# Optimization experiments

Hardware: AMD Instinct MI355X
Metric: run time of the kernel (lower is better)

## Reference

```python
import jax, jax.numpy as jnp
import numpy as np

N = 50000          # nodes
E = 1600000        # edges (avg degree 32)
B = 64             # graphs in batch
D_NODE = 128
D_EDGE = 64
D_EMB = 128
D_HID = 2 * D_EMB  # GCN output channels
EPS = 1e-5


def setup_inputs() -> dict:
    key = jax.random.key(0)
    ks = jax.random.split(key, 12)
    g = lambda k, shape: jax.random.normal(k, shape, jnp.float32) * (shape[0] ** -0.5)
    return {
        "x": jax.random.normal(ks[0], (N, D_NODE), jnp.float32),
        "edge_attr": jax.random.normal(ks[1], (E, D_EDGE), jnp.float32),
        "edge_index": jax.random.randint(ks[2], (2, E), 0, N),
        "batch": jnp.sort(jax.random.randint(ks[3], (N,), 0, B)),
        # GCNConv params
        "W1": g(ks[4], (D_NODE, D_HID)), "b1": jnp.zeros((D_HID,), jnp.float32),
        # TransformerConv params (heads=1)
        "Wq": g(ks[5], (D_HID, D_EMB)), "bq": jnp.zeros((D_EMB,), jnp.float32),
        "Wk": g(ks[6], (D_HID, D_EMB)), "bk": jnp.zeros((D_EMB,), jnp.float32),
        "Wv": g(ks[7], (D_HID, D_EMB)), "bv": jnp.zeros((D_EMB,), jnp.float32),
        "We": g(ks[8], (D_EDGE, D_EMB)), "be": jnp.zeros((D_EMB,), jnp.float32),
        "Wr": g(ks[9], (D_HID, D_EMB)), "br": jnp.zeros((D_EMB,), jnp.float32),
        # LayerNorm params
        "gamma": jnp.ones((D_EMB,), jnp.float32), "beta": jnp.zeros((D_EMB,), jnp.float32),
    }


def _forward(x, edge_attr, edge_index, batch,
             W1, b1, Wq, bq, Wk, bk, Wv, bv, We, be, Wr, br, gamma, beta):
    src, dst = edge_index[0], edge_index[1]

    # ---- GCNConv: symmetric normalization with self-loops ----
    xw = x @ W1                                                # [N, D_HID]
    deg = 1.0 + jax.ops.segment_sum(jnp.ones((E,), x.dtype), dst, num_segments=N)
    dinv = jax.lax.rsqrt(deg)                                  # deg >= 1
    norm = dinv[src] * dinv[dst]                               # [E]
    agg = jax.ops.segment_sum(xw[src] * norm[:, None], dst, num_segments=N)
    h = agg + xw * (dinv * dinv)[:, None] + b1                 # self-loop term
    h = jax.nn.relu(h)                                         # dropout = identity (eval)

    # ---- TransformerConv (heads=1, edge_dim) ----
    q = h @ Wq + bq                                            # [N, D_EMB]
    k = h @ Wk + bk
    v = h @ Wv + bv
    e = edge_attr @ We + be                                    # [E, D_EMB]
    k_j = k[src] + e
    v_j = v[src] + e
    logits = jnp.sum(q[dst] * k_j, axis=-1) / jnp.sqrt(jnp.float32(D_EMB))  # [E]
    # segment softmax over incoming edges of each target node
    lmax = jax.ops.segment_max(logits, dst, num_segments=N)
    exp_l = jnp.exp(logits - lmax[dst])
    denom = jax.ops.segment_sum(exp_l, dst, num_segments=N)
    alpha = exp_l / denom[dst]                                 # [E]
    out = jax.ops.segment_sum(alpha[:, None] * v_j, dst, num_segments=N)
    out = out + h @ Wr + br                                    # root/skip connection

    # ---- LayerNorm + ReLU ----
    mu = jnp.mean(out, axis=-1, keepdims=True)
    var = jnp.var(out, axis=-1, keepdims=True)
    out = (out - mu) * jax.lax.rsqrt(var + EPS) * gamma + beta
    out = jax.nn.relu(out)

    # ---- global mean pool over graphs ----
    sums = jax.ops.segment_sum(out, batch, num_segments=B)     # [B, D_EMB]
    cnts = jax.ops.segment_sum(jnp.ones((N,), out.dtype), batch, num_segments=B)
    return sums / jnp.maximum(cnts, 1.0)[:, None]


def reference(x, edge_attr, edge_index, batch,
              W1, b1, Wq, bq, Wk, bk, Wv, bv, We, be, Wr, br, gamma, beta):
    return _forward(x, edge_attr, edge_index, batch,
                    W1, b1, Wq, bq, Wk, bk, Wv, bv, We, be, Wr, br, gamma, beta)
```

## Files before the change

kernel.cpp:

```cpp
#include <hip/hip_runtime.h>

typedef short bf16x8 __attribute__((ext_vector_type(8)));
typedef float f32x4 __attribute__((ext_vector_type(4)));

#define DN 128
#define DE 64
#define DEMB 128
#define DHID 256
#define SCALE 0.08838834764831845f

__device__ __forceinline__ ushort f2bf(float f) {
  unsigned u = __float_as_uint(f);
  return (ushort)((u + 0x7FFFu + ((u >> 16) & 1u)) >> 16);
}
__device__ __forceinline__ float bf2f(ushort u) {
  return __uint_as_float((unsigned)u << 16);
}

__global__ void k_prep1(const float* __restrict__ W1, ushort* __restrict__ Wp1) {
  int idx = blockIdx.x * 256 + threadIdx.x;
  if (idx >= 16 * 4 * 64 * 8) return;
  int j = idx & 7, lane = (idx >> 3) & 63, s = (idx >> 9) & 3, t = idx >> 11;
  int k = s * 32 + (lane >> 4) * 8 + j;
  int c = t * 16 + (lane & 15);
  Wp1[idx] = f2bf(W1[k * DHID + c]);
}

__global__ void k_prep2(const float* __restrict__ Wq, const float* __restrict__ Wk,
                        const float* __restrict__ Wv, const float* __restrict__ Wr,
                        const float* __restrict__ We, ushort* __restrict__ Wp2) {
  int idx = blockIdx.x * 256 + threadIdx.x;
  if (idx >= 36 * 8 * 64 * 8) return;
  int j = idx & 7, lane = (idx >> 3) & 63, s = (idx >> 9) & 7, t = idx >> 12;
  int k = s * 32 + (lane >> 4) * 8 + j;
  int c = t * 16 + (lane & 15);
  float v;
  if (c < 128)       v = Wq[k * DEMB + c] * SCALE;
  else if (c < 256)  v = Wk[k * DEMB + (c - 128)];
  else if (c < 384)  v = Wv[k * DEMB + (c - 256)];
  else if (c < 512)  v = Wr[k * DEMB + (c - 384)];
  else {
    int cc = c - 512;
    float a = 0.f;
    for (int u = 0; u < DEMB; ++u) a += Wq[k * DEMB + u] * We[cc * DEMB + u];
    v = a * SCALE;
  }
  Wp2[idx] = f2bf(v);
}

__global__ void k_prep_b(const float* __restrict__ bq, const float* __restrict__ bk,
                         const float* __restrict__ bv, const float* __restrict__ br,
                         const float* __restrict__ be, const float* __restrict__ We,
                         float* __restrict__ bcat) {
  int j = blockIdx.x * 256 + threadIdx.x;
  if (j >= 576) return;
  float v;
  if (j < 128)       v = bq[j] * SCALE;
  else if (j < 256)  v = bk[j - 128] + be[j - 128];
  else if (j < 384)  v = bv[j - 256] + be[j - 256];
  else if (j < 512)  v = br[j - 384];
  else {
    int cc = j - 512;
    float a = 0.f;
    for (int u = 0; u < DEMB; ++u) a += bq[u] * We[cc * DEMB + u];
    v = a * SCALE;
  }
  bcat[j] = v;
}

__global__ void k_prep3(const float* __restrict__ We, ushort* __restrict__ Wp3) {
  int idx = blockIdx.x * 256 + threadIdx.x;
  if (idx >= 8 * 2 * 64 * 8) return;
  int j = idx & 7, lane = (idx >> 3) & 63, s = (idx >> 9) & 1, t = idx >> 10;
  int k = s * 32 + (lane >> 4) * 8 + j;
  int c = t * 16 + (lane & 15);
  Wp3[idx] = f2bf(We[k * DEMB + c]);
}

__global__ void k_deg(const int* __restrict__ ei, int* __restrict__ degi, int nE) {
  int e = blockIdx.x * 256 + threadIdx.x;
  if (e < nE) atomicAdd(&degi[ei[nE + e]], 1);
}

__global__ void k_dinv(const int* __restrict__ degi, float* __restrict__ dinv, int nN) {
  int n = blockIdx.x * 256 + threadIdx.x;
  if (n < nN) dinv[n] = rsqrtf(1.0f + (float)degi[n]);
}

__global__ __launch_bounds__(1024) void k_scan(const int* __restrict__ degi,
                                               int* __restrict__ row_ptr, int n) {
  __shared__ int wsum[16];
  __shared__ int carry_s;
  int lane = threadIdx.x & 63, wid = threadIdx.x >> 6;
  if (threadIdx.x == 0) carry_s = 0;
  __syncthreads();
  for (int base = 0; base < n; base += 1024) {
    int i = base + threadIdx.x;
    int v = (i < n) ? degi[i] : 0;
    int sc = v;
    #pragma unroll
    for (int off = 1; off < 64; off <<= 1) {
      int t = __shfl_up(sc, off);
      if (lane >= off) sc += t;
    }
    if (lane == 63) wsum[wid] = sc;
    int carry0 = carry_s;
    __syncthreads();
    if (wid == 0) {
      int w = (lane < 16) ? wsum[lane] : 0;
      int swc = w;
      #pragma unroll
      for (int off = 1; off < 16; off <<= 1) {
        int t = __shfl_up(swc, off);
        if (lane >= off) swc += t;
      }
      if (lane < 16) wsum[lane] = swc - w;
      if (lane == 15) carry_s = carry0 + swc;
    }
    __syncthreads();
    if (i < n) row_ptr[i] = carry0 + wsum[wid] + sc - v;
    __syncthreads();
  }
  if (threadIdx.x == 0) row_ptr[n] = carry_s;
}

__global__ void k_scatter(const int* __restrict__ ei, const int* __restrict__ row_ptr,
                          int* __restrict__ cursor, int2* __restrict__ csr_se, int nE) {
  int e = blockIdx.x * 256 + threadIdx.x;
  if (e >= nE) return;
  int dst = ei[nE + e];
  int pos = row_ptr[dst] + atomicAdd(&cursor[dst], 1);
  csr_se[pos] = make_int2(ei[e], e);
}

__global__ void k_gbounds(const int* __restrict__ batch, int* __restrict__ gstart,
                          int nN, int B) {
  int n = blockIdx.x * 256 + threadIdx.x;
  if (n >= nN) return;
  int b = batch[n];
  if (n == 0) {
    for (int g = 0; g <= b; ++g) gstart[g] = 0;
  } else {
    int pb = batch[n - 1];
    for (int g = pb + 1; g <= b; ++g) gstart[g] = n;
  }
  if (n == nN - 1) {
    for (int g = b + 1; g <= B; ++g) gstart[g] = nN;
  }
}

__global__ __launch_bounds__(256) void k_gemm1(const float* __restrict__ x,
                                               const ushort* __restrict__ Wp1,
                                               const float* __restrict__ dinv,
                                               ushort* __restrict__ xwsb, int nN) {
  int lane = threadIdx.x & 63, wave = threadIdx.x >> 6;
  int l15 = lane & 15, lh = lane >> 4;
  int m0 = blockIdx.x * 16;
  int rowa = m0 + l15; if (rowa >= nN) rowa = nN - 1;
  f32x4 acc[4] = {};
  for (int s = 0; s < 4; ++s) {
    const float* ap = &x[(size_t)rowa * DN + s * 32 + lh * 8];
    float4 a0 = *(const float4*)ap;
    float4 a1 = *(const float4*)(ap + 4);
    bf16x8 af;
    af[0] = (short)f2bf(a0.x); af[1] = (short)f2bf(a0.y);
    af[2] = (short)f2bf(a0.z); af[3] = (short)f2bf(a0.w);
    af[4] = (short)f2bf(a1.x); af[5] = (short)f2bf(a1.y);
    af[6] = (short)f2bf(a1.z); af[7] = (short)f2bf(a1.w);
    #pragma unroll
    for (int tt = 0; tt < 4; ++tt) {
      int t = wave * 4 + tt;
      bf16x8 bf = *(const bf16x8*)&Wp1[((t * 4 + s) * 64 + lane) * 8];
      acc[tt] = __builtin_amdgcn_mfma_f32_16x16x32_bf16(af, bf, acc[tt], 0, 0, 0);
    }
  }
  #pragma unroll
  for (int tt = 0; tt < 4; ++tt) {
    int c = (wave * 4 + tt) * 16 + l15;
    #pragma unroll
    for (int r = 0; r < 4; ++r) {
      int row = m0 + lh * 4 + r;
      if (row < nN) xwsb[(size_t)row * DHID + c] = f2bf(acc[tt][r] * dinv[row]);
    }
  }
}

__global__ __launch_bounds__(256) void k_gemm2(const ushort* __restrict__ hb,
                                               const ushort* __restrict__ Wp2,
                                               const float* __restrict__ bcat,
                                               ushort* __restrict__ qwb,
                                               ushort* __restrict__ kb,
                                               ushort* __restrict__ vb,
                                               ushort* __restrict__ hrb, int nN) {
  int lane = threadIdx.x & 63, wave = threadIdx.x >> 6;
  int l15 = lane & 15, lh = lane >> 4;
  int m0 = blockIdx.x * 16;
  int rowa = m0 + l15; if (rowa >= nN) rowa = nN - 1;
  f32x4 acc[9] = {};
  for (int s = 0; s < 8; ++s) {
    bf16x8 af = *(const bf16x8*)&hb[(size_t)rowa * DHID + s * 32 + lh * 8];
    #pragma unroll
    for (int tt = 0; tt < 9; ++tt) {
      int t = wave * 9 + tt;
      bf16x8 bf = *(const bf16x8*)&Wp2[((t * 8 + s) * 64 + lane) * 8];
      acc[tt] = __builtin_amdgcn_mfma_f32_16x16x32_bf16(af, bf, acc[tt], 0, 0, 0);
    }
  }
  #pragma unroll
  for (int tt = 0; tt < 9; ++tt) {
    int c = (wave * 9 + tt) * 16 + l15;
    float bc = bcat[c];
    #pragma unroll
    for (int r = 0; r < 4; ++r) {
      int row = m0 + lh * 4 + r;
      if (row >= nN) continue;
      ushort val = f2bf(acc[tt][r] + bc);
      if (c < 128)      qwb[(size_t)row * 192 + c] = val;
      else if (c < 256) kb[(size_t)row * 128 + (c - 128)] = val;
      else if (c < 384) vb[(size_t)row * 128 + (c - 256)] = val;
      else if (c < 512) hrb[(size_t)row * 128 + (c - 384)] = val;
      else              qwb[(size_t)row * 192 + 128 + (c - 512)] = val;
    }
  }
}

__global__ __launch_bounds__(256) void k_gcnE(const ushort* __restrict__ xwsb,
                                              const int2* __restrict__ csr_se,
                                              const int* __restrict__ row_ptr,
                                              const float* __restrict__ dinv,
                                              const float* __restrict__ b1,
                                              ushort* __restrict__ hb, int nN) {
  int lane = threadIdx.x & 63;
  int n = blockIdx.x * 4 + (threadIdx.x >> 6);
  if (n >= nN) return;
  int grp = lane >> 4, l15 = lane & 15;
  int beg = row_ptr[n], end = row_ptr[n + 1];
  float acc[16] = {};
  for (int i0 = beg; i0 < end; i0 += 8) {
    #pragma unroll
    for (int u = 0; u < 2; ++u) {
      int e = i0 + u * 4 + grp;
      bool val = e < end;
      int cl = val ? e : end - 1;
      int src = csr_se[cl].x;
      const ushort* xr = &xwsb[(size_t)src * DHID + l15 * 16];
      uint4 xa = *(const uint4*)xr;
      uint4 xb = *(const uint4*)(xr + 8);
      float w = val ? 1.f : 0.f;
      unsigned qq[8] = {xa.x, xa.y, xa.z, xa.w, xb.x, xb.y, xb.z, xb.w};
      #pragma unroll
      for (int d = 0; d < 8; ++d) {
        acc[2*d]   = fmaf(w, __uint_as_float(qq[d] << 16), acc[2*d]);
        acc[2*d+1] = fmaf(w, __uint_as_float(qq[d] & 0xFFFF0000u), acc[2*d+1]);
      }
    }
  }
  #pragma unroll
  for (int d = 0; d < 16; ++d) {
    acc[d] += __shfl_xor(acc[d], 16);
    acc[d] += __shfl_xor(acc[d], 32);
  }
  if (grp == 0) {
    const ushort* sr = &xwsb[(size_t)n * DHID + l15 * 16];
    uint4 sa = *(const uint4*)sr;
    uint4 sb = *(const uint4*)(sr + 8);
    unsigned sq[8] = {sa.x, sa.y, sa.z, sa.w, sb.x, sb.y, sb.z, sb.w};
    float dn = dinv[n];
    unsigned ov[8];
    #pragma unroll
    for (int d = 0; d < 8; ++d) {
      float blo = b1[l15 * 16 + 2*d], bhi = b1[l15 * 16 + 2*d + 1];
      float lo = __uint_as_float(sq[d] << 16);
      float hi = __uint_as_float(sq[d] & 0xFFFF0000u);
      float v0 = fmaxf((acc[2*d]   + lo) * dn + blo, 0.f);
      float v1 = fmaxf((acc[2*d+1] + hi) * dn + bhi, 0.f);
      ov[d] = (unsigned)f2bf(v0) | ((unsigned)f2bf(v1) << 16);
    }
    uint4 o0 = {ov[0], ov[1], ov[2], ov[3]};
    uint4 o1 = {ov[4], ov[5], ov[6], ov[7]};
    ushort* hr = &hb[(size_t)n * DHID + l15 * 16];
    *(uint4*)hr = o0;
    *(uint4*)(hr + 8) = o1;
  }
}

__global__ __launch_bounds__(256) void k_edge(const ushort* __restrict__ qwb,
                                              const ushort* __restrict__ kb,
                                              const ushort* __restrict__ vb,
                                              const float* __restrict__ ea32,
                                              const int2* __restrict__ csr_se,
                                              const int* __restrict__ row_ptr,
                                              float* __restrict__ sden,
                                              float* __restrict__ vaccf,
                                              ushort* __restrict__ ewb, int nN) {
  int lane = threadIdx.x & 63;
  int n = blockIdx.x * 4 + (threadIdx.x >> 6);
  if (n >= nN) return;
  int grp = lane >> 4, l15 = lane & 15;
  const ushort* qp = &qwb[(size_t)n * 192];
  bf16x8 qv = *(const bf16x8*)&qp[l15 * 8];
  ushort4 wv = *(const ushort4*)&qp[128 + l15 * 4];
  float q[8];
  #pragma unroll
  for (int d = 0; d < 8; ++d) q[d] = bf2f((ushort)qv[d]);
  float w0 = bf2f(wv.x), w1 = bf2f(wv.y), w2 = bf2f(wv.z), w3 = bf2f(wv.w);
  float s_acc = 0.f;
  float av[8] = {};
  float ae[4] = {};
  int beg = row_ptr[n], end = row_ptr[n + 1];
  for (int i0 = beg; i0 < end; i0 += 8) {
    #pragma unroll
    for (int u = 0; u < 2; ++u) {
      int e = i0 + u * 4 + grp;
      bool val = e < end;
      int cl = val ? e : end - 1;
      int2 se = csr_se[cl];
      bf16x8 kv8 = *(const bf16x8*)&kb[(size_t)se.x * 128 + l15 * 8];
      bf16x8 vv8 = *(const bf16x8*)&vb[(size_t)se.x * 128 + l15 * 8];
      float4 eav = *(const float4*)&ea32[(size_t)se.y * DE + l15 * 4];
      float dot = w0 * eav.x + w1 * eav.y + w2 * eav.z + w3 * eav.w;
      #pragma unroll
      for (int d = 0; d < 8; ++d) dot = fmaf(q[d], bf2f((ushort)kv8[d]), dot);
      dot += __shfl_xor(dot, 1);
      dot += __shfl_xor(dot, 2);
      dot += __shfl_xor(dot, 4);
      dot += __shfl_xor(dot, 8);
      float p = val ? __expf(dot) : 0.f;
      s_acc += p;
      #pragma unroll
      for (int d = 0; d < 8; ++d) av[d] = fmaf(p, bf2f((ushort)vv8[d]), av[d]);
      ae[0] = fmaf(p, eav.x, ae[0]);
      ae[1] = fmaf(p, eav.y, ae[1]);
      ae[2] = fmaf(p, eav.z, ae[2]);
      ae[3] = fmaf(p, eav.w, ae[3]);
    }
  }
  s_acc += __shfl_xor(s_acc, 16); s_acc += __shfl_xor(s_acc, 32);
  #pragma unroll
  for (int d = 0; d < 8; ++d) {
    av[d] += __shfl_xor(av[d], 16);
    av[d] += __shfl_xor(av[d], 32);
  }
  #pragma unroll
  for (int d = 0; d < 4; ++d) {
    ae[d] += __shfl_xor(ae[d], 16);
    ae[d] += __shfl_xor(ae[d], 32);
  }
  if (grp == 0) {
    if (l15 == 0) sden[n] = s_acc;
    float4 o0 = {av[0], av[1], av[2], av[3]};
    float4 o1 = {av[4], av[5], av[6], av[7]};
    float* vr = &vaccf[(size_t)n * 128 + l15 * 8];
    *(float4*)vr = o0;
    *(float4*)(vr + 4) = o1;
    ushort4 eo;
    eo.x = f2bf(ae[0]); eo.y = f2bf(ae[1]); eo.z = f2bf(ae[2]); eo.w = f2bf(ae[3]);
    *(ushort4*)&ewb[(size_t)n * DE + l15 * 4] = eo;
  }
}

__global__ __launch_bounds__(256) void k_ewe(const ushort* __restrict__ ewb,
                                             const ushort* __restrict__ Wp3,
                                             float* __restrict__ ewout, int nN) {
  int lane = threadIdx.x & 63, wave = threadIdx.x >> 6;
  int l15 = lane & 15, lh = lane >> 4;
  int m0 = blockIdx.x * 16;
  int rowa = m0 + l15; if (rowa >= nN) rowa = nN - 1;
  f32x4 acc[2] = {};
  #pragma unroll
  for (int s = 0; s < 2; ++s) {
    bf16x8 af = *(const bf16x8*)&ewb[(size_t)rowa * DE + s * 32 + lh * 8];
    #pragma unroll
    for (int tt = 0; tt < 2; ++tt) {
      int t = wave * 2 + tt;
      bf16x8 bf = *(const bf16x8*)&Wp3[((t * 2 + s) * 64 + lane) * 8];
      acc[tt] = __builtin_amdgcn_mfma_f32_16x16x32_bf16(af, bf, acc[tt], 0, 0, 0);
    }
  }
  #pragma unroll
  for (int tt = 0; tt < 2; ++tt) {
    int c = (wave * 2 + tt) * 16 + l15;
    #pragma unroll
    for (int r = 0; r < 4; ++r) {
      int row = m0 + lh * 4 + r;
      if (row < nN) ewout[(size_t)row * 128 + c] = acc[tt][r];
    }
  }
}

__global__ __launch_bounds__(256) void k_fin(const float* __restrict__ sden,
                                             const float* __restrict__ vaccf,
                                             const float* __restrict__ ewout,
                                             const ushort* __restrict__ hrb,
                                             const float* __restrict__ gamma,
                                             const float* __restrict__ beta,
                                             float* __restrict__ ynorm, int nN) {
  int lane = threadIdx.x & 63, grp = lane >> 5, l5 = lane & 31;
  int n = blockIdx.x * 8 + (threadIdx.x >> 6) * 2 + grp;
  if (n >= nN) return;
  float s = sden[n];
  float inv = (s > 0.f) ? 1.f / s : 0.f;
  float4 v4 = *(const float4*)&vaccf[(size_t)n * 128 + l5 * 4];
  float4 w4 = *(const float4*)&ewout[(size_t)n * 128 + l5 * 4];
  ushort4 hv = *(const ushort4*)&hrb[(size_t)n * 128 + l5 * 4];
  float4 o4;
  o4.x = (v4.x + w4.x) * inv + bf2f(hv.x);
  o4.y = (v4.y + w4.y) * inv + bf2f(hv.y);
  o4.z = (v4.z + w4.z) * inv + bf2f(hv.z);
  o4.w = (v4.w + w4.w) * inv + bf2f(hv.w);
  float s1 = o4.x + o4.y + o4.z + o4.w;
  float sq = o4.x*o4.x + o4.y*o4.y + o4.z*o4.z + o4.w*o4.w;
  #pragma unroll
  for (int off = 1; off < 32; off <<= 1) {
    s1 += __shfl_xor(s1, off);
    sq += __shfl_xor(sq, off);
  }
  float mu = s1 * (1.f / 128.f);
  float var = sq * (1.f / 128.f) - mu * mu;
  float rstd = rsqrtf(var + 1e-5f);
  float4 g4 = *(const float4*)&gamma[l5 * 4];
  float4 b4 = *(const float4*)&beta[l5 * 4];
  float4 y;
  y.x = fmaxf((o4.x - mu) * rstd * g4.x + b4.x, 0.f);
  y.y = fmaxf((o4.y - mu) * rstd * g4.y + b4.y, 0.f);
  y.z = fmaxf((o4.z - mu) * rstd * g4.z + b4.z, 0.f);
  y.w = fmaxf((o4.w - mu) * rstd * g4.w + b4.w, 0.f);
  *(float4*)&ynorm[(size_t)n * 128 + l5 * 4] = y;
}

__global__ __launch_bounds__(128) void k_pool(const float* __restrict__ ynorm,
                                              const int* __restrict__ gstart,
                                              float* __restrict__ out) {
  int b = blockIdx.x, t = threadIdx.x;
  int beg = gstart[b], end = gstart[b + 1];
  float a0 = 0.f, a1 = 0.f, a2 = 0.f, a3 = 0.f;
  int n = beg;
  for (; n + 4 <= end; n += 4) {
    a0 += ynorm[(size_t)(n + 0) * 128 + t];
    a1 += ynorm[(size_t)(n + 1) * 128 + t];
    a2 += ynorm[(size_t)(n + 2) * 128 + t];
    a3 += ynorm[(size_t)(n + 3) * 128 + t];
  }
  for (; n < end; ++n) a0 += ynorm[(size_t)n * 128 + t];
  float acc = (a0 + a1) + (a2 + a3);
  out[b * 128 + t] = acc / fmaxf((float)(end - beg), 1.f);
}

extern "C" void kernel_launch(void* const* d_in, const int* in_sizes, int n_in,
                              void* d_out, int out_size, void* d_ws, size_t ws_size,
                              hipStream_t stream) {
  const float* x         = (const float*)d_in[0];
  const float* edge_attr = (const float*)d_in[1];
  const int*   edge_index= (const int*)d_in[2];
  const int*   batch     = (const int*)d_in[3];
  const float* W1 = (const float*)d_in[4];
  const float* b1 = (const float*)d_in[5];
  const float* Wq = (const float*)d_in[6];  const float* bq = (const float*)d_in[7];
  const float* Wk = (const float*)d_in[8];  const float* bk = (const float*)d_in[9];
  const float* Wv = (const float*)d_in[10]; const float* bv = (const float*)d_in[11];
  const float* We = (const float*)d_in[12]; const float* be = (const float*)d_in[13];
  const float* Wr = (const float*)d_in[14]; const float* br = (const float*)d_in[15];
  const float* gamma = (const float*)d_in[16];
  const float* beta  = (const float*)d_in[17];
  float* out = (float*)d_out;

  const int nN = in_sizes[0] / DN;
  const int nE = in_sizes[1] / DE;
  const int B  = out_size / DEMB;

  char* p = (char*)d_ws;
  auto alloc = [&](size_t bytes) -> void* {
    void* r = (void*)p;
    p += (bytes + 255) & ~(size_t)255;
    return r;
  };
  int*   degi   = (int*)  alloc((size_t)nN * 4);
  int*   cursor = (int*)  alloc((size_t)nN * 4);
  size_t zero_bytes = (size_t)(p - (char*)d_ws);
  int*    row_ptr = (int*)   alloc((size_t)(nN + 1) * 4);
  int*    gstart  = (int*)   alloc((size_t)(B + 1) * 4);
  float*  dinv    = (float*) alloc((size_t)nN * 4);
  int2*   csr_se  = (int2*)  alloc((size_t)nE * 8);
  ushort* Wp1     = (ushort*)alloc((size_t)16 * 4 * 64 * 8 * 2);
  ushort* Wp2     = (ushort*)alloc((size_t)36 * 8 * 64 * 8 * 2);
  ushort* Wp3     = (ushort*)alloc((size_t)8 * 2 * 64 * 8 * 2);
  float*  bcat    = (float*) alloc(576 * 4);
  ushort* qwb     = (ushort*)alloc((size_t)nN * 192 * 2);
  ushort* hrb     = (ushort*)alloc((size_t)nN * 128 * 2);
  ushort* hb      = (ushort*)alloc((size_t)nN * DHID * 2);
  ushort* xwsb    = (ushort*)alloc((size_t)nN * DHID * 2);
  ushort* kb      = xwsb;
  ushort* vb      = xwsb + (size_t)nN * 128;
  float*  sden    = (float*) alloc((size_t)nN * 4);
  float*  vaccf   = (float*) alloc((size_t)nN * 128 * 4);
  ushort* ewb     = (ushort*)alloc((size_t)nN * DE * 2);
  float*  ewout   = (float*) alloc((size_t)nN * 128 * 4);
  float*  ynorm   = (float*) alloc((size_t)nN * 128 * 4);
  size_t required = (size_t)(p - (char*)d_ws);
  if (ws_size < required) return;

  hipMemsetAsync(d_ws, 0, zero_bytes, stream);

  k_prep1<<<128, 256, 0, stream>>>(W1, Wp1);
  k_prep2<<<576, 256, 0, stream>>>(Wq, Wk, Wv, Wr, We, Wp2);
  k_prep_b<<<3, 256, 0, stream>>>(bq, bk, bv, br, be, We, bcat);
  k_prep3<<<32, 256, 0, stream>>>(We, Wp3);
  k_deg<<<(nE + 255) / 256, 256, 0, stream>>>(edge_index, degi, nE);
  k_dinv<<<(nN + 255) / 256, 256, 0, stream>>>(degi, dinv, nN);
  k_scan<<<1, 1024, 0, stream>>>(degi, row_ptr, nN);
  k_scatter<<<(nE + 255) / 256, 256, 0, stream>>>(edge_index, row_ptr, cursor,
                                                  csr_se, nE);
  k_gbounds<<<(nN + 255) / 256, 256, 0, stream>>>(batch, gstart, nN, B);
  k_gemm1<<<(nN + 15) / 16, 256, 0, stream>>>(x, Wp1, dinv, xwsb, nN);
  k_gcnE<<<(nN + 3) / 4, 256, 0, stream>>>(xwsb, csr_se, row_ptr, dinv, b1, hb, nN);
  k_gemm2<<<(nN + 15) / 16, 256, 0, stream>>>(hb, Wp2, bcat, qwb, kb, vb, hrb, nN);
  k_edge<<<(nN + 3) / 4, 256, 0, stream>>>(qwb, kb, vb, edge_attr, csr_se, row_ptr,
                                           sden, vaccf, ewb, nN);
  k_ewe<<<(nN + 15) / 16, 256, 0, stream>>>(ewb, Wp3, ewout, nN);
  k_fin<<<(nN + 7) / 8, 256, 0, stream>>>(sden, vaccf, ewout, hrb, gamma, beta,
                                          ynorm, nN);
  k_pool<<<B, 128, 0, stream>>>(ynorm, gstart, out);
}
```

Measured before the change: 680.8 us.

## Aggregate GCN neighbors on 128-dim inputs before the W1 GEMM

```diff
diff --git a/kernel.cpp b/kernel.cpp
--- a/kernel.cpp
+++ b/kernel.cpp
@@ -149,24 +149,85 @@
   }
 }
 
-__global__ __launch_bounds__(256) void k_gemm1(const float* __restrict__ x,
-                                               const ushort* __restrict__ Wp1,
+__global__ __launch_bounds__(256) void k_xcast(const float* __restrict__ x,
                                                const float* __restrict__ dinv,
-                                               ushort* __restrict__ xwsb, int nN) {
+                                               ushort* __restrict__ xsb, int nN) {
+  int idx = blockIdx.x * 256 + threadIdx.x;
+  if (idx >= nN * 32) return;
+  int n = idx >> 5, q = idx & 31;
+  float dn = dinv[n];
+  float4 v = *(const float4*)&x[(size_t)n * DN + q * 4];
+  ushort4 o;
+  o.x = f2bf(v.x * dn); o.y = f2bf(v.y * dn);
+  o.z = f2bf(v.z * dn); o.w = f2bf(v.w * dn);
+  *(ushort4*)&xsb[(size_t)n * DN + q * 4] = o;
+}
+
+__global__ __launch_bounds__(256) void k_gcnX(const ushort* __restrict__ xsb,
+                                              const int2* __restrict__ csr_se,
+                                              const int* __restrict__ row_ptr,
+                                              const float* __restrict__ dinv,
+                                              ushort* __restrict__ aggxb, int nN) {
+  int lane = threadIdx.x & 63;
+  int n = blockIdx.x * 4 + (threadIdx.x >> 6);
+  if (n >= nN) return;
+  int grp = lane >> 4, l15 = lane & 15;
+  int beg = row_ptr[n], end = row_ptr[n + 1];
+  float acc[8] = {};
+  for (int i0 = beg; i0 < end; i0 += 16) {
+    #pragma unroll
+    for (int u = 0; u < 4; ++u) {
+      int e = i0 + u * 4 + grp;
+      bool val = e < end;
+      int cl = val ? e : end - 1;
+      int src = csr_se[cl].x;
+      uint4 xa = *(const uint4*)&xsb[(size_t)src * DN + l15 * 8];
+      float w = val ? 1.f : 0.f;
+      unsigned qq[4] = {xa.x, xa.y, xa.z, xa.w};
+      #pragma unroll
+      for (int d = 0; d < 4; ++d) {
+        acc[2*d]   = fmaf(w, __uint_as_float(qq[d] << 16), acc[2*d]);
+        acc[2*d+1] = fmaf(w, __uint_as_float(qq[d] & 0xFFFF0000u), acc[2*d+1]);
+      }
+    }
+  }
+  #pragma unroll
+  for (int d = 0; d < 8; ++d) {
+    acc[d] += __shfl_xor(acc[d], 16);
+    acc[d] += __shfl_xor(acc[d], 32);
+  }
+  if (grp == 0) {
+    uint4 sa = *(const uint4*)&xsb[(size_t)n * DN + l15 * 8];
+    unsigned sq[4] = {sa.x, sa.y, sa.z, sa.w};
+    float dn = dinv[n];
+    ushort o[8];
+    #pragma unroll
+    for (int d = 0; d < 4; ++d) {
+      float lo = __uint_as_float(sq[d] << 16);
+      float hi = __uint_as_float(sq[d] & 0xFFFF0000u);
+      o[2*d]   = f2bf(dn * (acc[2*d]   + lo));
+      o[2*d+1] = f2bf(dn * (acc[2*d+1] + hi));
+    }
+    uint4 ov = {(unsigned)o[0] | ((unsigned)o[1] << 16),
+                (unsigned)o[2] | ((unsigned)o[3] << 16),
+                (unsigned)o[4] | ((unsigned)o[5] << 16),
+                (unsigned)o[6] | ((unsigned)o[7] << 16)};
+    *(uint4*)&aggxb[(size_t)n * DN + l15 * 8] = ov;
+  }
+}
+
+__global__ __launch_bounds__(256) void k_gemm1b(const ushort* __restrict__ aggxb,
+                                                const ushort* __restrict__ Wp1,
+                                                const float* __restrict__ b1,
+                                                ushort* __restrict__ hb, int nN) {
   int lane = threadIdx.x & 63, wave = threadIdx.x >> 6;
   int l15 = lane & 15, lh = lane >> 4;
   int m0 = blockIdx.x * 16;
   int rowa = m0 + l15; if (rowa >= nN) rowa = nN - 1;
   f32x4 acc[4] = {};
+  #pragma unroll
   for (int s = 0; s < 4; ++s) {
-    const float* ap = &x[(size_t)rowa * DN + s * 32 + lh * 8];
-    float4 a0 = *(const float4*)ap;
-    float4 a1 = *(const float4*)(ap + 4);
-    bf16x8 af;
-    af[0] = (short)f2bf(a0.x); af[1] = (short)f2bf(a0.y);
-    af[2] = (short)f2bf(a0.z); af[3] = (short)f2bf(a0.w);
-    af[4] = (short)f2bf(a1.x); af[5] = (short)f2bf(a1.y);
-    af[6] = (short)f2bf(a1.z); af[7] = (short)f2bf(a1.w);
+    bf16x8 af = *(const bf16x8*)&aggxb[(size_t)rowa * DN + s * 32 + lh * 8];
     #pragma unroll
     for (int tt = 0; tt < 4; ++tt) {
       int t = wave * 4 + tt;
@@ -177,10 +238,11 @@
   #pragma unroll
   for (int tt = 0; tt < 4; ++tt) {
     int c = (wave * 4 + tt) * 16 + l15;
+    float bc = b1[c];
     #pragma unroll
     for (int r = 0; r < 4; ++r) {
       int row = m0 + lh * 4 + r;
-      if (row < nN) xwsb[(size_t)row * DHID + c] = f2bf(acc[tt][r] * dinv[row]);
+      if (row < nN) hb[(size_t)row * DHID + c] = f2bf(fmaxf(acc[tt][r] + bc, 0.f));
     }
   }
 }
@@ -221,66 +283,6 @@
       else if (c < 512) hrb[(size_t)row * 128 + (c - 384)] = val;
       else              qwb[(size_t)row * 192 + 128 + (c - 512)] = val;
     }
-  }
-}
-
-__global__ __launch_bounds__(256) void k_gcnE(const ushort* __restrict__ xwsb,
-                                              const int2* __restrict__ csr_se,
-                                              const int* __restrict__ row_ptr,
-                                              const float* __restrict__ dinv,
-                                              const float* __restrict__ b1,
-                                              ushort* __restrict__ hb, int nN) {
-  int lane = threadIdx.x & 63;
-  int n = blockIdx.x * 4 + (threadIdx.x >> 6);
-  if (n >= nN) return;
-  int grp = lane >> 4, l15 = lane & 15;
-  int beg = row_ptr[n], end = row_ptr[n + 1];
-  float acc[16] = {};
-  for (int i0 = beg; i0 < end; i0 += 8) {
-    #pragma unroll
-    for (int u = 0; u < 2; ++u) {
-      int e = i0 + u * 4 + grp;
-      bool val = e < end;
-      int cl = val ? e : end - 1;
-      int src = csr_se[cl].x;
-      const ushort* xr = &xwsb[(size_t)src * DHID + l15 * 16];
-      uint4 xa = *(const uint4*)xr;
-      uint4 xb = *(const uint4*)(xr + 8);
-      float w = val ? 1.f : 0.f;
-      unsigned qq[8] = {xa.x, xa.y, xa.z, xa.w, xb.x, xb.y, xb.z, xb.w};
-      #pragma unroll
-      for (int d = 0; d < 8; ++d) {
-        acc[2*d]   = fmaf(w, __uint_as_float(qq[d] << 16), acc[2*d]);
-        acc[2*d+1] = fmaf(w, __uint_as_float(qq[d] & 0xFFFF0000u), acc[2*d+1]);
-      }
-    }
-  }
-  #pragma unroll
-  for (int d = 0; d < 16; ++d) {
-    acc[d] += __shfl_xor(acc[d], 16);
-    acc[d] += __shfl_xor(acc[d], 32);
-  }
-  if (grp == 0) {
-    const ushort* sr = &xwsb[(size_t)n * DHID + l15 * 16];
-    uint4 sa = *(const uint4*)sr;
-    uint4 sb = *(const uint4*)(sr + 8);
-    unsigned sq[8] = {sa.x, sa.y, sa.z, sa.w, sb.x, sb.y, sb.z, sb.w};
-    float dn = dinv[n];
-    unsigned ov[8];
-    #pragma unroll
-    for (int d = 0; d < 8; ++d) {
-      float blo = b1[l15 * 16 + 2*d], bhi = b1[l15 * 16 + 2*d + 1];
-      float lo = __uint_as_float(sq[d] << 16);
-      float hi = __uint_as_float(sq[d] & 0xFFFF0000u);
-      float v0 = fmaxf((acc[2*d]   + lo) * dn + blo, 0.f);
-      float v1 = fmaxf((acc[2*d+1] + hi) * dn + bhi, 0.f);
-      ov[d] = (unsigned)f2bf(v0) | ((unsigned)f2bf(v1) << 16);
-    }
-    uint4 o0 = {ov[0], ov[1], ov[2], ov[3]};
-    uint4 o1 = {ov[4], ov[5], ov[6], ov[7]};
-    ushort* hr = &hb[(size_t)n * DHID + l15 * 16];
-    *(uint4*)hr = o0;
-    *(uint4*)(hr + 8) = o1;
   }
 }
 
@@ -308,31 +310,38 @@
   float av[8] = {};
   float ae[4] = {};
   int beg = row_ptr[n], end = row_ptr[n + 1];
-  for (int i0 = beg; i0 < end; i0 += 8) {
-    #pragma unroll
-    for (int u = 0; u < 2; ++u) {
+  for (int i0 = beg; i0 < end; i0 += 16) {
+    int2 se[4]; bool vl[4];
+    #pragma unroll
+    for (int u = 0; u < 4; ++u) {
       int e = i0 + u * 4 + grp;
-      bool val = e < end;
-      int cl = val ? e : end - 1;
-      int2 se = csr_se[cl];
-      bf16x8 kv8 = *(const bf16x8*)&kb[(size_t)se.x * 128 + l15 * 8];
-      bf16x8 vv8 = *(const bf16x8*)&vb[(size_t)se.x * 128 + l15 * 8];
-      float4 eav = *(const float4*)&ea32[(size_t)se.y * DE + l15 * 4];
-      float dot = w0 * eav.x + w1 * eav.y + w2 * eav.z + w3 * eav.w;
+      vl[u] = e < end;
+      se[u] = csr_se[vl[u] ? e : end - 1];
+    }
+    bf16x8 kv8[4]; bf16x8 vv8[4]; float4 eav[4];
+    #pragma unroll
+    for (int u = 0; u < 4; ++u) {
+      kv8[u] = *(const bf16x8*)&kb[(size_t)se[u].x * 128 + l15 * 8];
+      vv8[u] = *(const bf16x8*)&vb[(size_t)se[u].x * 128 + l15 * 8];
+      eav[u] = *(const float4*)&ea32[(size_t)se[u].y * DE + l15 * 4];
+    }
+    #pragma unroll
+    for (int u = 0; u < 4; ++u) {
+      float dot = w0 * eav[u].x + w1 * eav[u].y + w2 * eav[u].z + w3 * eav[u].w;
       #pragma unroll
-      for (int d = 0; d < 8; ++d) dot = fmaf(q[d], bf2f((ushort)kv8[d]), dot);
+      for (int d = 0; d < 8; ++d) dot = fmaf(q[d], bf2f((ushort)kv8[u][d]), dot);
       dot += __shfl_xor(dot, 1);
       dot += __shfl_xor(dot, 2);
       dot += __shfl_xor(dot, 4);
       dot += __shfl_xor(dot, 8);
-      float p = val ? __expf(dot) : 0.f;
+      float p = vl[u] ? __expf(dot) : 0.f;
       s_acc += p;
       #pragma unroll
-      for (int d = 0; d < 8; ++d) av[d] = fmaf(p, bf2f((ushort)vv8[d]), av[d]);
-      ae[0] = fmaf(p, eav.x, ae[0]);
-      ae[1] = fmaf(p, eav.y, ae[1]);
-      ae[2] = fmaf(p, eav.z, ae[2]);
-      ae[3] = fmaf(p, eav.w, ae[3]);
+      for (int d = 0; d < 8; ++d) av[d] = fmaf(p, bf2f((ushort)vv8[u][d]), av[d]);
+      ae[0] = fmaf(p, eav[u].x, ae[0]);
+      ae[1] = fmaf(p, eav[u].y, ae[1]);
+      ae[2] = fmaf(p, eav[u].z, ae[2]);
+      ae[3] = fmaf(p, eav[u].w, ae[3]);
     }
   }
   s_acc += __shfl_xor(s_acc, 16); s_acc += __shfl_xor(s_acc, 32);
@@ -488,9 +497,10 @@
   ushort* qwb     = (ushort*)alloc((size_t)nN * 192 * 2);
   ushort* hrb     = (ushort*)alloc((size_t)nN * 128 * 2);
   ushort* hb      = (ushort*)alloc((size_t)nN * DHID * 2);
-  ushort* xwsb    = (ushort*)alloc((size_t)nN * DHID * 2);
-  ushort* kb      = xwsb;
-  ushort* vb      = xwsb + (size_t)nN * 128;
+  ushort* xsb     = (ushort*)alloc((size_t)nN * DN * 2);
+  ushort* aggxb   = (ushort*)alloc((size_t)nN * DN * 2);
+  ushort* kb      = xsb;
+  ushort* vb      = aggxb;
   float*  sden    = (float*) alloc((size_t)nN * 4);
   float*  vaccf   = (float*) alloc((size_t)nN * 128 * 4);
   ushort* ewb     = (ushort*)alloc((size_t)nN * DE * 2);
@@ -511,8 +521,9 @@
   k_scatter<<<(nE + 255) / 256, 256, 0, stream>>>(edge_index, row_ptr, cursor,
                                                   csr_se, nE);
   k_gbounds<<<(nN + 255) / 256, 256, 0, stream>>>(batch, gstart, nN, B);
-  k_gemm1<<<(nN + 15) / 16, 256, 0, stream>>>(x, Wp1, dinv, xwsb, nN);
-  k_gcnE<<<(nN + 3) / 4, 256, 0, stream>>>(xwsb, csr_se, row_ptr, dinv, b1, hb, nN);
+  k_xcast<<<(nN * 32 + 255) / 256, 256, 0, stream>>>(x, dinv, xsb, nN);
+  k_gcnX<<<(nN + 3) / 4, 256, 0, stream>>>(xsb, csr_se, row_ptr, dinv, aggxb, nN);
+  k_gemm1b<<<(nN + 15) / 16, 256, 0, stream>>>(aggxb, Wp1, b1, hb, nN);
   k_gemm2<<<(nN + 15) / 16, 256, 0, stream>>>(hb, Wp2, bcat, qwb, kb, vb, hrb, nN);
   k_edge<<<(nN + 3) / 4, 256, 0, stream>>>(qwb, kb, vb, edge_attr, csr_se, row_ptr,
                                            sden, vaccf, ewb, nN);
```

New measurement: 661.2 us. 1.03x faster.
